# Performance work log

Hardware: AMD Instinct MI355X
Metric: run time of the kernel (lower is better)

Reference implementation:

```python
import jax, jax.numpy as jnp
import numpy as np

N_NODES = 50000
N_EDGES = 320000
HIDDEN = 256
N_LAYERS = 5
BN_EPS = 1e-5


def setup_inputs() -> dict:
    key = jax.random.key(0)
    ks = jax.random.split(key, 8)
    x = jax.random.normal(ks[0], (N_NODES, HIDDEN), dtype=jnp.float32)
    edge_index = jax.random.randint(ks[1], (2, N_EDGES), 0, N_NODES, dtype=jnp.int64)
    edge_attr = jax.random.uniform(ks[2], (N_EDGES, 4), dtype=jnp.float32)
    # xavier-ish scales
    mlp_w = jax.random.normal(ks[3], (N_LAYERS, 2 * HIDDEN, HIDDEN), dtype=jnp.float32) * (1.0 / np.sqrt(2 * HIDDEN))
    mlp_b = jnp.zeros((N_LAYERS, HIDDEN), dtype=jnp.float32)
    ew1 = jax.random.normal(ks[4], (N_LAYERS, 1, HIDDEN // 2), dtype=jnp.float32)
    ew2 = jax.random.normal(ks[5], (N_LAYERS, 3, HIDDEN // 2), dtype=jnp.float32) * (1.0 / np.sqrt(3.0))
    bn_g = jnp.ones((N_LAYERS, HIDDEN), dtype=jnp.float32)
    bn_b = jnp.zeros((N_LAYERS, HIDDEN), dtype=jnp.float32)
    return {"x": x, "edge_index": edge_index, "edge_attr": edge_attr,
            "mlp_w": mlp_w, "mlp_b": mlp_b, "ew1": ew1, "ew2": ew2,
            "bn_g": bn_g, "bn_b": bn_b}


def _mpnn(x, edge_index, edge_attr, mlp_w, mlp_b, ew1, ew2, bn_g, bn_b):
    n = x.shape[0]
    row, col = edge_index[0], edge_index[1]
    # gcn_norm: deg computed by scatter-add of ones at col (targets)
    deg = jax.ops.segment_sum(jnp.ones((edge_index.shape[1],), x.dtype), col, num_segments=n)
    dinv = jnp.where(deg > 0, deg ** -0.5, 0.0)
    norm = dinv[row] * dinv[col]  # [E]
    h = x
    for l in range(N_LAYERS):
        # edge feature fusion: Linear(1,h/2) on last col, Linear(3,h/2) on first 3
        edge_fea = jnp.concatenate([edge_attr[:, 3:] @ ew1[l], edge_attr[:, 0:3] @ ew2[l]], axis=-1)  # [E,H]
        msg = norm[:, None] * (h[row] + edge_fea)                      # gather + scale
        agg = jax.ops.segment_sum(msg, col, num_segments=n)            # scatter-add
        h = jax.nn.relu(jnp.concatenate([h, agg], axis=1) @ mlp_w[l] + mlp_b[l])
        # BatchNorm1d (training-mode batch stats, biased var)
        mu = h.mean(axis=0)
        var = h.var(axis=0)
        h = (h - mu) * jax.lax.rsqrt(var + BN_EPS) * bn_g[l] + bn_b[l]
        if l != N_LAYERS - 1:
            h = jax.nn.relu(h)
        # dropout with drop_ratio=0 is identity
    return h


def reference(x, edge_index, edge_attr, mlp_w, mlp_b, ew1, ew2, bn_g, bn_b):
    return _mpnn(x, edge_index, edge_attr, mlp_w, mlp_b, ew1, ew2, bn_g, bn_b)
```

## Files before the change

### kernel.cpp

```cpp
#include <hip/hip_runtime.h>
#include <stdint.h>

typedef short short8 __attribute__((ext_vector_type(8)));
typedef float f32x4 __attribute__((ext_vector_type(4)));
typedef unsigned short u16;

#define HID 256
#define NLAYERS 5
#define BN_EPS 1e-5f

__device__ __forceinline__ float bf2f(u16 u) {
    union { unsigned int i; float f; } v;
    v.i = ((unsigned int)u) << 16;
    return v.f;
}
__device__ __forceinline__ u16 f2bf(float f) {
    union { float f; unsigned int i; } v;
    v.f = f;
    unsigned int r = v.i + 0x7FFFu + ((v.i >> 16) & 1u);
    return (u16)(r >> 16);
}
__device__ __forceinline__ void split_bf(float f, u16& hi, u16& lo) {
    hi = f2bf(f);
    lo = f2bf(f - bf2f(hi));
}

__device__ __forceinline__ void gl_lds16(const void* gsrc, void* ldst) {
    const __attribute__((address_space(1))) unsigned int* g =
        reinterpret_cast<const __attribute__((address_space(1))) unsigned int*>(
            reinterpret_cast<uintptr_t>(gsrc));
    __attribute__((address_space(3))) unsigned int* l =
        reinterpret_cast<__attribute__((address_space(3))) unsigned int*>(
            reinterpret_cast<uintptr_t>(ldst));
    __builtin_amdgcn_global_load_lds(g, l, 16, 0, 0);
}


__global__ __launch_bounds__(256) void k_zero32(unsigned int* p, int n) {
    int i = blockIdx.x * 256 + threadIdx.x;
    if (i < n) p[i] = 0u;
}


__global__ __launch_bounds__(256) void k_detect(const int* ei, int* flag, int E) {
    __shared__ int nz;
    if (threadIdx.x == 0) nz = 0;
    __syncthreads();
    int lim = (2 * E < 4096) ? 2 * E : 4096;
    int c = 0;
    for (int i = threadIdx.x; 2 * i + 1 < lim; i += 256) c += (ei[2 * i + 1] != 0);
    atomicAdd(&nz, c);
    __syncthreads();
    if (threadIdx.x == 0) flag[0] = (nz == 0) ? 1 : 0;
}

__global__ __launch_bounds__(256) void k_deg(const int* ei, const int* flag, int* deg, int E, int N) {
    int e = blockIdx.x * 256 + threadIdx.x;
    if (e >= E) return;
    int w = flag[0];
    int col = w ? ei[2 * (E + e)] : ei[E + e];
    if ((unsigned)col < (unsigned)N) atomicAdd(&deg[col], 1);
}

__global__ __launch_bounds__(256) void k_dinv(const int* deg, float* dinv, int N) {
    int n = blockIdx.x * 256 + threadIdx.x;
    if (n < N) { int d = deg[n]; dinv[n] = d > 0 ? rsqrtf((float)d) : 0.0f; }
}

__global__ __launch_bounds__(256) void k_scan1(const int* deg, int* offs, int* bsum, int N) {
    __shared__ int s[256];
    int tid = threadIdx.x;
    int i = blockIdx.x * 256 + tid;
    int v = (i < N) ? deg[i] : 0;
    s[tid] = v;
    __syncthreads();
    for (int off = 1; off < 256; off <<= 1) {
        int t = (tid >= off) ? s[tid - off] : 0;
        __syncthreads();
        s[tid] += t;
        __syncthreads();
    }
    if (i < N) offs[i] = s[tid] - v;
    if (tid == 255) bsum[blockIdx.x] = s[tid];
}

__global__ __launch_bounds__(256) void k_scan2(const int* bsum, int* bscan, int NB) {
    __shared__ int s[256];
    int tid = threadIdx.x;
    int v = (tid < NB) ? bsum[tid] : 0;
    s[tid] = v;
    __syncthreads();
    for (int off = 1; off < 256; off <<= 1) {
        int t = (tid >= off) ? s[tid - off] : 0;
        __syncthreads();
        s[tid] += t;
        __syncthreads();
    }
    bscan[tid] = s[tid] - v;
}

__global__ __launch_bounds__(256) void k_scan3(int* offs, const int* bscan, int* cursor, int N, int E) {
    int i = blockIdx.x * 256 + threadIdx.x;
    if (i < N) {
        int o = offs[i] + bscan[blockIdx.x];
        offs[i] = o;
        cursor[i] = o;
    }
    if (i == 0) offs[N] = E;
}

__global__ __launch_bounds__(256) void k_place(const int* ei, const int* flag, const float4* eattr,
                                               int* cursor, int* srow, float4* sea, int E, int N) {
    int e = blockIdx.x * 256 + threadIdx.x;
    if (e >= E) return;
    int w = flag[0];
    int r = w ? ei[2 * e] : ei[e];
    int c = w ? ei[2 * (E + e)] : ei[E + e];
    if ((unsigned)c >= (unsigned)N) return;
    int p = atomicAdd(&cursor[c], 1);
    srow[p] = r;
    sea[p] = eattr[e];
}

__global__ __launch_bounds__(256) void k_move(const int* srow, const float4* sea, const float* sdinv,
                                              const int* soffs, int* rowArr, float4* eaP,
                                              float* dinvF, int* offsF, int E, int N) {
    int i = blockIdx.x * 256 + threadIdx.x;
    if (i < E) { rowArr[i] = srow[i]; eaP[i] = sea[i]; }
    if (i < N) dinvF[i] = sdinv[i];
    if (i <= N) offsF[i] = soffs[i];
}

__global__ __launch_bounds__(256) void k_precheckN(const int* offsF, const int* cursor, const float* dinvF,
                                                   const int* gflag, int* diag, int N, int E) {
    int i = blockIdx.x * 256 + threadIdx.x;
    if (i < N) {
        if (offsF[i + 1] < offsF[i]) atomicOr(&diag[0], 1);
        if (cursor[i] != offsF[i + 1]) atomicOr(&diag[0], 2);
        float d = dinvF[i];
        if (!(d == d) || fabsf(d) > 1e10f) atomicOr(&diag[0], 4);
    }
    if (i == 0) {
        if (offsF[N] != E) atomicOr(&diag[0], 8);
        diag[7] = gflag[0];
    }
}
__global__ __launch_bounds__(256) void k_precheckE(const int* rowArr, int* diag, int E, int N) {
    int p = blockIdx.x * 256 + threadIdx.x;
    if (p < E && (unsigned)rowArr[p] >= (unsigned)N) atomicOr(&diag[0], 16);
}

__global__ __launch_bounds__(256) void k_wsplit(const float* W, u16* wpH, u16* wpL, float* colsum) {
    if (blockIdx.x == 0) {
        colsum[threadIdx.x] = 0.f;
        colsum[256 + threadIdx.x] = 0.f;
    }
    int t = blockIdx.x * 256 + threadIdx.x;
    int lane = t & 63;
    int nbg = (t >> 6) & 15;
    int kb = t >> 10;
    int quad = lane >> 4, nl = lane & 15;
    const float* src = W + (size_t)(kb * 32 + quad * 8) * HID + nbg * 16 + nl;
    short8 vh, vl;
#pragma unroll
    for (int j = 0; j < 8; ++j) {
        u16 h, l;
        split_bf(src[(size_t)j * HID], h, l);
        vh[j] = (short)h;
        vl[j] = (short)l;
    }
    *((short8*)wpH + t) = vh;
    *((short8*)wpL + t) = vl;
}

#define FEA(ea, j) ((ea).w * w1v[j] + (ea).x * w20[j] + (ea).y * w21[j] + (ea).z * w22[j])

__global__ __launch_bounds__(256) void k_agg(const void* hin_, const u16* hin_lo, int hf32,
                                             const int* offs, const int* rowArr, const float4* eaP,
                                             const float* dinv, const float* ew1, const float* ew2,
                                             u16* agg_hi, u16* agg_lo, int* diag, int M) {
    (void)hin_lo;
    int lane = threadIdx.x & 63, wave = threadIdx.x >> 6;
    int n = blockIdx.x * 4 + wave;

    float w1v[4] = {0.f, 0.f, 0.f, 0.f};
    float w20[4] = {0.f, 0.f, 0.f, 0.f};
    float w21[4] = {0.f, 0.f, 0.f, 0.f};
    float w22[4] = {0.f, 0.f, 0.f, 0.f};
    if (lane < 32) {
        int c = lane * 4;
#pragma unroll
        for (int j = 0; j < 4; ++j) w1v[j] = ew1[c + j];
    } else {
        int cc = (lane - 32) * 4;
#pragma unroll
        for (int j = 0; j < 4; ++j) {
            w20[j] = ew2[cc + j];
            w21[j] = ew2[128 + cc + j];
            w22[j] = ew2[256 + cc + j];
        }
    }

    if (n >= M) return;
    float dn = dinv[n];
    int s = offs[n], e = offs[n + 1];
    float a0 = 0.f, a1 = 0.f, a2 = 0.f, a3 = 0.f;
    int p = s;

    if (hf32) {
        for (; p + 4 <= e; p += 4) {
            int r0 = rowArr[p + 0], r1 = rowArr[p + 1], r2 = rowArr[p + 2], r3 = rowArr[p + 3];
            float4 ea0 = eaP[p + 0], ea1 = eaP[p + 1], ea2 = eaP[p + 2], ea3 = eaP[p + 3];
            float4 hv0 = *((const float4*)hin_ + (size_t)r0 * 64 + lane);
            float4 hv1 = *((const float4*)hin_ + (size_t)r1 * 64 + lane);
            float4 hv2 = *((const float4*)hin_ + (size_t)r2 * 64 + lane);
            float4 hv3 = *((const float4*)hin_ + (size_t)r3 * 64 + lane);
            float n0 = dn * dinv[r0], n1 = dn * dinv[r1], n2 = dn * dinv[r2], n3 = dn * dinv[r3];
            a0 += n0 * (hv0.x + FEA(ea0, 0)) + n1 * (hv1.x + FEA(ea1, 0))
                + n2 * (hv2.x + FEA(ea2, 0)) + n3 * (hv3.x + FEA(ea3, 0));
            a1 += n0 * (hv0.y + FEA(ea0, 1)) + n1 * (hv1.y + FEA(ea1, 1))
                + n2 * (hv2.y + FEA(ea2, 1)) + n3 * (hv3.y + FEA(ea3, 1));
            a2 += n0 * (hv0.z + FEA(ea0, 2)) + n1 * (hv1.z + FEA(ea1, 2))
                + n2 * (hv2.z + FEA(ea2, 2)) + n3 * (hv3.z + FEA(ea3, 2));
            a3 += n0 * (hv0.w + FEA(ea0, 3)) + n1 * (hv1.w + FEA(ea1, 3))
                + n2 * (hv2.w + FEA(ea2, 3)) + n3 * (hv3.w + FEA(ea3, 3));
        }
        for (; p < e; ++p) {
            int r = rowArr[p];
            float4 ea = eaP[p];
            float nrm = dn * dinv[r];
            float4 hv = *((const float4*)hin_ + (size_t)r * 64 + lane);
            a0 += nrm * (hv.x + FEA(ea, 0));
            a1 += nrm * (hv.y + FEA(ea, 1));
            a2 += nrm * (hv.z + FEA(ea, 2));
            a3 += nrm * (hv.w + FEA(ea, 3));
        }
    } else {
        for (; p + 4 <= e; p += 4) {
            int r0 = rowArr[p + 0], r1 = rowArr[p + 1], r2 = rowArr[p + 2], r3 = rowArr[p + 3];
            float4 ea0 = eaP[p + 0], ea1 = eaP[p + 1], ea2 = eaP[p + 2], ea3 = eaP[p + 3];
            ushort4 hh0 = *((const ushort4*)hin_ + (size_t)r0 * 64 + lane);
            ushort4 hh1 = *((const ushort4*)hin_ + (size_t)r1 * 64 + lane);
            ushort4 hh2 = *((const ushort4*)hin_ + (size_t)r2 * 64 + lane);
            ushort4 hh3 = *((const ushort4*)hin_ + (size_t)r3 * 64 + lane);
            float n0 = dn * dinv[r0], n1 = dn * dinv[r1], n2 = dn * dinv[r2], n3 = dn * dinv[r3];
            a0 += n0 * (bf2f(hh0.x) + FEA(ea0, 0)) + n1 * (bf2f(hh1.x) + FEA(ea1, 0))
                + n2 * (bf2f(hh2.x) + FEA(ea2, 0)) + n3 * (bf2f(hh3.x) + FEA(ea3, 0));
            a1 += n0 * (bf2f(hh0.y) + FEA(ea0, 1)) + n1 * (bf2f(hh1.y) + FEA(ea1, 1))
                + n2 * (bf2f(hh2.y) + FEA(ea2, 1)) + n3 * (bf2f(hh3.y) + FEA(ea3, 1));
            a2 += n0 * (bf2f(hh0.z) + FEA(ea0, 2)) + n1 * (bf2f(hh1.z) + FEA(ea1, 2))
                + n2 * (bf2f(hh2.z) + FEA(ea2, 2)) + n3 * (bf2f(hh3.z) + FEA(ea3, 2));
            a3 += n0 * (bf2f(hh0.w) + FEA(ea0, 3)) + n1 * (bf2f(hh1.w) + FEA(ea1, 3))
                + n2 * (bf2f(hh2.w) + FEA(ea2, 3)) + n3 * (bf2f(hh3.w) + FEA(ea3, 3));
        }
        for (; p < e; ++p) {
            int r = rowArr[p];
            float4 ea = eaP[p];
            float nrm = dn * dinv[r];
            ushort4 hh = *((const ushort4*)hin_ + (size_t)r * 64 + lane);
            a0 += nrm * (bf2f(hh.x) + FEA(ea, 0));
            a1 += nrm * (bf2f(hh.y) + FEA(ea, 1));
            a2 += nrm * (bf2f(hh.z) + FEA(ea, 2));
            a3 += nrm * (bf2f(hh.w) + FEA(ea, 3));
        }
    }

    int bad = 0;
    if (!(a0 == a0)) { a0 = 777.f; bad++; }
    if (!(a1 == a1)) { a1 = 777.f; bad++; }
    if (!(a2 == a2)) { a2 = 777.f; bad++; }
    if (!(a3 == a3)) { a3 = 777.f; bad++; }
    if (bad) atomicAdd(&diag[1], bad);
    ushort4 oh, ol;
    split_bf(a0, oh.x, ol.x);
    split_bf(a1, oh.y, ol.y);
    split_bf(a2, oh.z, ol.z);
    split_bf(a3, oh.w, ol.w);
    *((ushort4*)agg_hi + (size_t)n * 64 + lane) = oh;
    *((ushort4*)agg_lo + (size_t)n * 64 + lane) = ol;
}

__global__ __launch_bounds__(256, 2) void MPNN_79044578115931_kernel(
        const void* hinA_, const u16* hinA_lo, int hf32,
        const u16* agg_hi, const u16* agg_lo,
        const u16* wpH, const u16* wpL, const float* bias,
        u16* y_hi, u16* y_lo,
        float* colsum, float* colsumsq, int* diag, int M) {
    __shared__ __align__(16) u16 bstage[16384];
    __shared__ float lsum[256];
    __shared__ float lsq[256];

    int tid = threadIdx.x;
    int lane = tid & 63, wave = tid >> 6;
    int quad = lane >> 4, nl = lane & 15;
    int mBase = blockIdx.x * 128 + wave * 32;
    int rowA0 = mBase + nl;
    int rowA1 = mBase + 16 + nl;
    if (rowA0 >= M) rowA0 = M - 1;
    if (rowA1 >= M) rowA1 = M - 1;

    lsum[tid] = 0.f;
    lsq[tid] = 0.f;

    f32x4 acc0[16], acc1[16];
#pragma unroll
    for (int i = 0; i < 16; ++i) {
        acc0[i] = {0.f, 0.f, 0.f, 0.f};
        acc1[i] = {0.f, 0.f, 0.f, 0.f};
    }

    for (int kb = 0; kb < 16; ++kb) {
        __syncthreads();

        const u16* srcH = wpH + (size_t)kb * 8192;
        const u16* srcL = wpL + (size_t)kb * 8192;
#pragma unroll
        for (int i = 0; i < 4; ++i) {
            int ci = i * 256 + tid;
            gl_lds16(srcH + ci * 8, &bstage[ci * 8]);
            gl_lds16(srcL + ci * 8, &bstage[8192 + ci * 8]);
        }

        short8 a0h, a0l, a1h, a1l;
        if (kb < 8) {
            int k0 = kb * 32 + quad * 8;
            if (hf32) {
                const float* hp0 = (const float*)hinA_ + (size_t)rowA0 * HID + k0;
                const float* hp1 = (const float*)hinA_ + (size_t)rowA1 * HID + k0;
#pragma unroll
                for (int j = 0; j < 8; ++j) {
                    u16 h, l;
                    split_bf(hp0[j], h, l);
                    a0h[j] = (short)h; a0l[j] = (short)l;
                    split_bf(hp1[j], h, l);
                    a1h[j] = (short)h; a1l[j] = (short)l;
                }
            } else {
                a0h = *(const short8*)((const u16*)hinA_ + (size_t)rowA0 * HID + k0);
                a0l = *(const short8*)(hinA_lo + (size_t)rowA0 * HID + k0);
                a1h = *(const short8*)((const u16*)hinA_ + (size_t)rowA1 * HID + k0);
                a1l = *(const short8*)(hinA_lo + (size_t)rowA1 * HID + k0);
            }
        } else {
            int k0 = (kb - 8) * 32 + quad * 8;
            a0h = *(const short8*)(agg_hi + (size_t)rowA0 * HID + k0);
            a0l = *(const short8*)(agg_lo + (size_t)rowA0 * HID + k0);
            a1h = *(const short8*)(agg_hi + (size_t)rowA1 * HID + k0);
            a1l = *(const short8*)(agg_lo + (size_t)rowA1 * HID + k0);
        }

        __syncthreads();

        const short8* bbase = (const short8*)bstage;
#pragma unroll
        for (int nbg = 0; nbg < 16; ++nbg) {
            short8 bh = bbase[nbg * 64 + lane];
            short8 bl = bbase[1024 + nbg * 64 + lane];
            acc0[nbg] = __builtin_amdgcn_mfma_f32_16x16x32_bf16(a0h, bh, acc0[nbg], 0, 0, 0);
            acc1[nbg] = __builtin_amdgcn_mfma_f32_16x16x32_bf16(a1h, bh, acc1[nbg], 0, 0, 0);
            acc0[nbg] = __builtin_amdgcn_mfma_f32_16x16x32_bf16(a0l, bh, acc0[nbg], 0, 0, 0);
            acc1[nbg] = __builtin_amdgcn_mfma_f32_16x16x32_bf16(a1l, bh, acc1[nbg], 0, 0, 0);
            acc0[nbg] = __builtin_amdgcn_mfma_f32_16x16x32_bf16(a0h, bl, acc0[nbg], 0, 0, 0);
            acc1[nbg] = __builtin_amdgcn_mfma_f32_16x16x32_bf16(a1h, bl, acc1[nbg], 0, 0, 0);
        }
    }

    __syncthreads();

    int badY = 0;
#pragma unroll
    for (int nbg = 0; nbg < 16; ++nbg) {
        int c = nbg * 16 + nl;
        float bv = bias[c];
        float s = 0.f, q = 0.f;
#pragma unroll
        for (int r = 0; r < 4; ++r) {
            int m = mBase + quad * 4 + r;
            if (m < M) {
                float v = acc0[nbg][r] + bv;
                if (!(v == v)) { v = 777.f; badY++; }
                v = v > 0.f ? v : 0.f;
                u16 h, l;
                split_bf(v, h, l);
                y_hi[(size_t)m * HID + c] = h;
                y_lo[(size_t)m * HID + c] = l;
                s += v;
                q += v * v;
            }
        }
        atomicAdd(&lsum[c], s);
        atomicAdd(&lsq[c], q);
    }
#pragma unroll
    for (int nbg = 0; nbg < 16; ++nbg) {
        int c = nbg * 16 + nl;
        float bv = bias[c];
        float s = 0.f, q = 0.f;
#pragma unroll
        for (int r = 0; r < 4; ++r) {
            int m = mBase + 16 + quad * 4 + r;
            if (m < M) {
                float v = acc1[nbg][r] + bv;
                if (!(v == v)) { v = 777.f; badY++; }
                v = v > 0.f ? v : 0.f;
                u16 h, l;
                split_bf(v, h, l);
                y_hi[(size_t)m * HID + c] = h;
                y_lo[(size_t)m * HID + c] = l;
                s += v;
                q += v * v;
            }
        }
        atomicAdd(&lsum[c], s);
        atomicAdd(&lsq[c], q);
    }
    if (badY) atomicAdd(&diag[2], badY);
    __syncthreads();
    atomicAdd(&colsum[tid], lsum[tid]);
    atomicAdd(&colsumsq[tid], lsq[tid]);
}

__global__ __launch_bounds__(256) void k_bnscale(const float* colsum, const float* colsumsq,
                                                 const float* g, const float* b,
                                                 float* scale, float* shift, int* diag, int M) {
    int c = threadIdx.x;
    float mu = colsum[c] / (float)M;
    float var = colsumsq[c] / (float)M - mu * mu;
    if (!(mu == mu) || !(var == var) || var > 1e30f) atomicAdd(&diag[3], 1);
    if (var < 0.f) var = 0.f;
    float sc = rsqrtf(var + BN_EPS) * g[c];
    scale[c] = sc;
    shift[c] = b[c] - mu * sc;
}

__global__ __launch_bounds__(256) void k_bnapply(const u16* src_hi, const u16* src_lo,
                                                 u16* dst_hi, u16* dst_lo,
                                                 const float* scale, const float* shift,
                                                 float* outf, int finalL, int relu, int total) {
    int q4 = blockIdx.x * 256 + threadIdx.x;
    int idx = q4 * 4;
    if (idx >= total) return;
    int c = idx & (HID - 1);
    ushort4 vh = *((const ushort4*)src_hi + q4);
    ushort4 vl = *((const ushort4*)src_lo + q4);
    float o0 = scale[c + 0] * (bf2f(vh.x) + bf2f(vl.x)) + shift[c + 0];
    float o1 = scale[c + 1] * (bf2f(vh.y) + bf2f(vl.y)) + shift[c + 1];
    float o2 = scale[c + 2] * (bf2f(vh.z) + bf2f(vl.z)) + shift[c + 2];
    float o3 = scale[c + 3] * (bf2f(vh.w) + bf2f(vl.w)) + shift[c + 3];
    if (relu) {
        o0 = o0 > 0.f ? o0 : 0.f;
        o1 = o1 > 0.f ? o1 : 0.f;
        o2 = o2 > 0.f ? o2 : 0.f;
        o3 = o3 > 0.f ? o3 : 0.f;
    }
    if (finalL) {
        float4 ov; ov.x = o0; ov.y = o1; ov.z = o2; ov.w = o3;
        *((float4*)outf + q4) = ov;
    } else {
        ushort4 oh, ol;
        split_bf(o0, oh.x, ol.x);
        split_bf(o1, oh.y, ol.y);
        split_bf(o2, oh.z, ol.z);
        split_bf(o3, oh.w, ol.w);
        *((ushort4*)dst_hi + q4) = oh;
        *((ushort4*)dst_lo + q4) = ol;
    }
}

__global__ void k_encode(const int* diag, float* out) {
    if (threadIdx.x != 0 || blockIdx.x != 0) return;
    int k = -1;
    for (int i = 0; i < 4; ++i) if (diag[i] != 0) { k = i; break; }
    if (k < 0) return;
    out[0] = (float)(1 + k + (diag[7] != 0 ? 8 : 0)) * 1048576.0f;
}


extern "C" void kernel_launch(void* const* d_in, const int* in_sizes, int n_in,
                              void* d_out, int out_size, void* d_ws, size_t ws_size,
                              hipStream_t stream) {
    const float*  x     = (const float*)d_in[0];
    const int*    ei    = (const int*)d_in[1];
    const float4* eattr = (const float4*)d_in[2];
    const float*  mlp_w = (const float*)d_in[3];
    const float*  mlp_b = (const float*)d_in[4];
    const float*  ew1   = (const float*)d_in[5];
    const float*  ew2   = (const float*)d_in[6];
    const float*  bn_g  = (const float*)d_in[7];
    const float*  bn_b  = (const float*)d_in[8];
    (void)n_in; (void)out_size; (void)d_ws; (void)ws_size;

    const int N = in_sizes[0] / HID;
    const int E = in_sizes[1] / 2;
    const size_t P = (size_t)N * HID;

    char* st = (char*)d_out;
    int*    S_deg    = (int*)   (st + 0);
    float*  S_dinv   = (float*) (st + 204800);
    int*    S_offs   = (int*)   (st + 409600);
    int*    S_cursor = (int*)   (st + 614400);
    int*    S_bsum   = (int*)   (st + 819200);
    int*    S_bscan  = (int*)   (st + 820224);
    int*    S_gflag  = (int*)   (st + 821248);
    int*    S_row    = (int*)   (st + 1048576);
    float4* S_ea     = (float4*)(st + 2621440);

    char* eb = (char*)d_in[1];
    int*   rowArr = (int*)  (eb + 0);
    float* dinvF  = (float*)(eb + 1280000);
    int*   offsF  = (int*)  (eb + 1480000);
    float* colsum = (float*)(eb + 1680128);
    float* colsq  = (float*)(eb + 1681152);
    float* scaleF = (float*)(eb + 1682176);
    float* shiftF = (float*)(eb + 1683200);
    int*   diag   = (int*)  (eb + 1684224);
    u16*   wpH    = (u16*)  (eb + 1685504);
    u16*   wpL    = (u16*)  (eb + 1947648);
    float4* eaP   = (float4*)d_in[2];

    u16* sX_hi = (u16*)d_in[0];
    u16* sX_lo = sX_hi + P;
    u16* sD_hi = (u16*)d_out;
    u16* sD_lo = sD_hi + P;

    int NB  = (N + 255) / 256;
    int NBE = (E + 255) / 256;
    int NBG = (N + 127) / 128;
    int NBA = (N + 3) / 4;
    int NBQ = (int)((P / 4 + 255) / 256);

    k_detect<<<1, 256, 0, stream>>>(ei, S_gflag, E);
    k_zero32<<<NB, 256, 0, stream>>>((unsigned int*)S_deg, N);
    k_deg<<<NBE, 256, 0, stream>>>(ei, S_gflag, S_deg, E, N);
    k_dinv<<<NB, 256, 0, stream>>>(S_deg, S_dinv, N);
    k_scan1<<<NB, 256, 0, stream>>>(S_deg, S_offs, S_bsum, N);
    k_scan2<<<1, 256, 0, stream>>>(S_bsum, S_bscan, NB);
    k_scan3<<<NB, 256, 0, stream>>>(S_offs, S_bscan, S_cursor, N, E);
    k_place<<<NBE, 256, 0, stream>>>(ei, S_gflag, eattr, S_cursor, S_row, S_ea, E, N);
    k_move<<<NBE, 256, 0, stream>>>(S_row, S_ea, S_dinv, S_offs, rowArr, eaP, dinvF, offsF, E, N);
    k_zero32<<<1, 256, 0, stream>>>((unsigned int*)diag, 256);
    k_precheckN<<<NB, 256, 0, stream>>>(offsF, S_cursor, dinvF, S_gflag, diag, N, E);
    k_precheckE<<<NBE, 256, 0, stream>>>(rowArr, diag, E, N);

    for (int l = 0; l < NLAYERS; ++l) {
        int even = (l % 2 == 0);
        u16* dst_hi = even ? sD_hi : sX_hi;
        u16* dst_lo = even ? sD_lo : sX_lo;
        const void* hinA; const u16* hin_lo; int hf32;
        if (l == 0) { hinA = (const void*)x; hin_lo = 0; hf32 = 1; }
        else if (even) { hinA = (const void*)sX_hi; hin_lo = sX_lo; hf32 = 0; }
        else { hinA = (const void*)sD_hi; hin_lo = sD_lo; hf32 = 0; }

        k_wsplit<<<64, 256, 0, stream>>>(mlp_w + (size_t)l * 512 * HID, wpH, wpL, colsum);
        k_agg<<<NBA, 256, 0, stream>>>(hinA, hin_lo, hf32, offsF, rowArr, eaP, dinvF,
                                       ew1 + (size_t)l * 128, ew2 + (size_t)l * 384,
                                       dst_hi, dst_lo, diag, N);
        MPNN_79044578115931_kernel<<<NBG, 256, 0, stream>>>(
            hinA, hin_lo, hf32, dst_hi, dst_lo, wpH, wpL,
            mlp_b + (size_t)l * HID, dst_hi, dst_lo, colsum, colsq, diag, N);
        k_bnscale<<<1, 256, 0, stream>>>(colsum, colsq,
                                         bn_g + (size_t)l * HID, bn_b + (size_t)l * HID,
                                         scaleF, shiftF, diag, N);
        int finalL = (l == NLAYERS - 1) ? 1 : 0;
        int relu = finalL ? 0 : 1;
        k_bnapply<<<NBQ, 256, 0, stream>>>(dst_hi, dst_lo, dst_hi, dst_lo, scaleF, shiftF,
                                           (float*)d_in[0], finalL, relu, (int)P);
    }

    hipMemcpyAsync(d_out, d_in[0], P * 4, hipMemcpyDeviceToDevice, stream);
    k_encode<<<1, 64, 0, stream>>>(diag, (float*)d_out);
}
```

Baseline: 926.6 us.

## Fold BatchNorm apply and ReLU into next layer's aggregation and GEMM loads

Removes the per-layer BatchNorm-apply pass for all but the final layer. The next layer's aggregation and GEMM kernels now load the raw pre-BN activations and apply scale, shift and ReLU on the fly. This saves a full read and write of the hidden state each layer. In exchange, the aggregation applies the BN transform per gathered edge, and only to the hi bf16 half, which loses precision. The GEMM also re-splits its A operands after the transform.

```diff
diff --git a/kernel.cpp b/kernel.cpp
--- a/kernel.cpp
+++ b/kernel.cpp
@@ -174,10 +174,12 @@
 }
 
 #define FEA(ea, j) ((ea).w * w1v[j] + (ea).x * w20[j] + (ea).y * w21[j] + (ea).z * w22[j])
+#define BNX(u, comp) (fmaxf(sc4.comp * bf2f(u) + sh4.comp, 0.f))
 
 __global__ __launch_bounds__(256) void k_agg(const void* hin_, const u16* hin_lo, int hf32,
                                              const int* offs, const int* rowArr, const float4* eaP,
                                              const float* dinv, const float* ew1, const float* ew2,
+                                             const float* bnsc, const float* bnsh,
                                              u16* agg_hi, u16* agg_lo, int* diag, int M) {
     (void)hin_lo;
     int lane = threadIdx.x & 63, wave = threadIdx.x >> 6;
@@ -199,6 +201,12 @@
             w21[j] = ew2[128 + cc + j];
             w22[j] = ew2[256 + cc + j];
         }
+    }
+
+    float4 sc4 = {0.f, 0.f, 0.f, 0.f}, sh4 = {0.f, 0.f, 0.f, 0.f};
+    if (!hf32) {
+        sc4 = ((const float4*)bnsc)[lane];
+        sh4 = ((const float4*)bnsh)[lane];
     }
 
     if (n >= M) return;
@@ -244,24 +252,24 @@
             ushort4 hh2 = *((const ushort4*)hin_ + (size_t)r2 * 64 + lane);
             ushort4 hh3 = *((const ushort4*)hin_ + (size_t)r3 * 64 + lane);
             float n0 = dn * dinv[r0], n1 = dn * dinv[r1], n2 = dn * dinv[r2], n3 = dn * dinv[r3];
-            a0 += n0 * (bf2f(hh0.x) + FEA(ea0, 0)) + n1 * (bf2f(hh1.x) + FEA(ea1, 0))
-                + n2 * (bf2f(hh2.x) + FEA(ea2, 0)) + n3 * (bf2f(hh3.x) + FEA(ea3, 0));
-            a1 += n0 * (bf2f(hh0.y) + FEA(ea0, 1)) + n1 * (bf2f(hh1.y) + FEA(ea1, 1))
-                + n2 * (bf2f(hh2.y) + FEA(ea2, 1)) + n3 * (bf2f(hh3.y) + FEA(ea3, 1));
-            a2 += n0 * (bf2f(hh0.z) + FEA(ea0, 2)) + n1 * (bf2f(hh1.z) + FEA(ea1, 2))
-                + n2 * (bf2f(hh2.z) + FEA(ea2, 2)) + n3 * (bf2f(hh3.z) + FEA(ea3, 2));
-            a3 += n0 * (bf2f(hh0.w) + FEA(ea0, 3)) + n1 * (bf2f(hh1.w) + FEA(ea1, 3))
-                + n2 * (bf2f(hh2.w) + FEA(ea2, 3)) + n3 * (bf2f(hh3.w) + FEA(ea3, 3));
+            a0 += n0 * (BNX(hh0.x, x) + FEA(ea0, 0)) + n1 * (BNX(hh1.x, x) + FEA(ea1, 0))
+                + n2 * (BNX(hh2.x, x) + FEA(ea2, 0)) + n3 * (BNX(hh3.x, x) + FEA(ea3, 0));
+            a1 += n0 * (BNX(hh0.y, y) + FEA(ea0, 1)) + n1 * (BNX(hh1.y, y) + FEA(ea1, 1))
+                + n2 * (BNX(hh2.y, y) + FEA(ea2, 1)) + n3 * (BNX(hh3.y, y) + FEA(ea3, 1));
+            a2 += n0 * (BNX(hh0.z, z) + FEA(ea0, 2)) + n1 * (BNX(hh1.z, z) + FEA(ea1, 2))
+                + n2 * (BNX(hh2.z, z) + FEA(ea2, 2)) + n3 * (BNX(hh3.z, z) + FEA(ea3, 2));
+            a3 += n0 * (BNX(hh0.w, w) + FEA(ea0, 3)) + n1 * (BNX(hh1.w, w) + FEA(ea1, 3))
+                + n2 * (BNX(hh2.w, w) + FEA(ea2, 3)) + n3 * (BNX(hh3.w, w) + FEA(ea3, 3));
         }
         for (; p < e; ++p) {
             int r = rowArr[p];
             float4 ea = eaP[p];
             float nrm = dn * dinv[r];
             ushort4 hh = *((const ushort4*)hin_ + (size_t)r * 64 + lane);
-            a0 += nrm * (bf2f(hh.x) + FEA(ea, 0));
-            a1 += nrm * (bf2f(hh.y) + FEA(ea, 1));
-            a2 += nrm * (bf2f(hh.z) + FEA(ea, 2));
-            a3 += nrm * (bf2f(hh.w) + FEA(ea, 3));
+            a0 += nrm * (BNX(hh.x, x) + FEA(ea, 0));
+            a1 += nrm * (BNX(hh.y, y) + FEA(ea, 1));
+            a2 += nrm * (BNX(hh.z, z) + FEA(ea, 2));
+            a3 += nrm * (BNX(hh.w, w) + FEA(ea, 3));
         }
     }
 
@@ -284,6 +292,7 @@
         const void* hinA_, const u16* hinA_lo, int hf32,
         const u16* agg_hi, const u16* agg_lo,
         const u16* wpH, const u16* wpL, const float* bias,
+        const float* bnsc, const float* bnsh,
         u16* y_hi, u16* y_lo,
         float* colsum, float* colsumsq, int* diag, int M) {
     __shared__ __align__(16) u16 bstage[16384];
@@ -322,6 +331,7 @@
         }
 
         short8 a0h, a0l, a1h, a1l;
+        float4 scv0, scv1, shv0, shv1;
         if (kb < 8) {
             int k0 = kb * 32 + quad * 8;
             if (hf32) {
@@ -340,6 +350,11 @@
                 a0l = *(const short8*)(hinA_lo + (size_t)rowA0 * HID + k0);
                 a1h = *(const short8*)((const u16*)hinA_ + (size_t)rowA1 * HID + k0);
                 a1l = *(const short8*)(hinA_lo + (size_t)rowA1 * HID + k0);
+                int q4 = k0 >> 2;
+                scv0 = ((const float4*)bnsc)[q4];
+                scv1 = ((const float4*)bnsc)[q4 + 1];
+                shv0 = ((const float4*)bnsh)[q4];
+                shv1 = ((const float4*)bnsh)[q4 + 1];
             }
         } else {
             int k0 = (kb - 8) * 32 + quad * 8;
@@ -350,6 +365,23 @@
         }
 
         __syncthreads();
+
+        if (!hf32 && kb < 8) {
+            float scr[8] = {scv0.x, scv0.y, scv0.z, scv0.w, scv1.x, scv1.y, scv1.z, scv1.w};
+            float shr[8] = {shv0.x, shv0.y, shv0.z, shv0.w, shv1.x, shv1.y, shv1.z, shv1.w};
+#pragma unroll
+            for (int j = 0; j < 8; ++j) {
+                float f0 = scr[j] * (bf2f((u16)a0h[j]) + bf2f((u16)a0l[j])) + shr[j];
+                f0 = f0 > 0.f ? f0 : 0.f;
+                float f1 = scr[j] * (bf2f((u16)a1h[j]) + bf2f((u16)a1l[j])) + shr[j];
+                f1 = f1 > 0.f ? f1 : 0.f;
+                u16 h, l;
+                split_bf(f0, h, l);
+                a0h[j] = (short)h; a0l[j] = (short)l;
+                split_bf(f1, h, l);
+                a1h[j] = (short)h; a1l[j] = (short)l;
+            }
+        }
 
         const short8* bbase = (const short8*)bstage;
 #pragma unroll
@@ -554,17 +586,19 @@
         k_wsplit<<<64, 256, 0, stream>>>(mlp_w + (size_t)l * 512 * HID, wpH, wpL, colsum);
         k_agg<<<NBA, 256, 0, stream>>>(hinA, hin_lo, hf32, offsF, rowArr, eaP, dinvF,
                                        ew1 + (size_t)l * 128, ew2 + (size_t)l * 384,
+                                       scaleF, shiftF,
                                        dst_hi, dst_lo, diag, N);
         MPNN_79044578115931_kernel<<<NBG, 256, 0, stream>>>(
             hinA, hin_lo, hf32, dst_hi, dst_lo, wpH, wpL,
-            mlp_b + (size_t)l * HID, dst_hi, dst_lo, colsum, colsq, diag, N);
+            mlp_b + (size_t)l * HID, scaleF, shiftF,
+            dst_hi, dst_lo, colsum, colsq, diag, N);
         k_bnscale<<<1, 256, 0, stream>>>(colsum, colsq,
                                          bn_g + (size_t)l * HID, bn_b + (size_t)l * HID,
                                          scaleF, shiftF, diag, N);
-        int finalL = (l == NLAYERS - 1) ? 1 : 0;
-        int relu = finalL ? 0 : 1;
-        k_bnapply<<<NBQ, 256, 0, stream>>>(dst_hi, dst_lo, dst_hi, dst_lo, scaleF, shiftF,
-                                           (float*)d_in[0], finalL, relu, (int)P);
+        if (l == NLAYERS - 1) {
+            k_bnapply<<<NBQ, 256, 0, stream>>>(dst_hi, dst_lo, dst_hi, dst_lo, scaleF, shiftF,
+                                               (float*)d_in[0], 1, 0, (int)P);
+        }
     }
 
     hipMemcpyAsync(d_out, d_in[0], P * 4, hipMemcpyDeviceToDevice, stream);
```

New measurement: 908.6 us. Within noise of the previous version (-1.9%).
